# Kernel optimization log

Hardware: AMD Instinct MI355X
Metric: run time of the kernel (lower is better)

Reference implementation:

```python
import jax, jax.numpy as jnp
import numpy as np
import math

B, C, H, W = 32, 384, 64, 64      # batch, backbone dim, feature-map HxW
E, NH = 256, 16                   # embed_dim, num_heads (grapsules per image)
HD = E // NH                      # head dim
RFF_HALF, HID = 32, 128           # RFF rows (out=64), GNN hidden


def setup_inputs() -> dict:
    key = jax.random.key(0)
    ks = jax.random.split(key, 10)
    rn = lambda k, s: (0.02 * jax.random.normal(k, s)).astype(jnp.float32)
    x = jax.random.normal(ks[0], (B, C, H, W), jnp.float32)
    qw = rn(ks[1], (E, C)); qb = jnp.zeros((E,), jnp.float32)
    kw = rn(ks[2], (E, C)); kb = jnp.zeros((E,), jnp.float32)
    vw = rn(ks[3], (E, C)); vb = jnp.zeros((E,), jnp.float32)
    # RFF B ~ N(0,1) * sigma * 2*pi, sigma=1.0
    B_rff = (jax.random.normal(ks[4], (RFF_HALF, 2)) * (2.0 * math.pi)).astype(jnp.float32)
    msg_w = rn(ks[5], (HID, E)); msg_b = jnp.zeros((HID,), jnp.float32)
    emb_w = rn(ks[6], (HID, 2 * RFF_HALF))
    lin1_w = rn(ks[7], (4 * HID, HID)); lin1_b = jnp.zeros((4 * HID,), jnp.float32)
    lin2_w = rn(ks[8], (E, 4 * HID)); lin2_b = jnp.zeros((E,), jnp.float32)
    layer_scale = jnp.full((1, E), 1e-6, jnp.float32)
    # fully-connected directed graph (no self loops) among the NH grapsules of each image
    pairs = np.array([(i, j) for i in range(NH) for j in range(NH) if i != j], dtype=np.int32)
    off = (np.arange(B, dtype=np.int32) * NH)[:, None]
    edge_src = jnp.asarray((pairs[:, 0][None, :] + off).reshape(-1))
    edge_dst = jnp.asarray((pairs[:, 1][None, :] + off).reshape(-1))
    return dict(x=x, qw=qw, qb=qb, kw=kw, kb=kb, vw=vw, vb=vb, B_rff=B_rff,
                msg_w=msg_w, msg_b=msg_b, emb_w=emb_w, lin1_w=lin1_w, lin1_b=lin1_b,
                lin2_w=lin2_w, lin2_b=lin2_b, layer_scale=layer_scale,
                edge_src=edge_src, edge_dst=edge_dst)


def _forward(x, qw, qb, kw, kb, vw, vb, B_rff, msg_w, msg_b, emb_w,
             lin1_w, lin1_b, lin2_w, lin2_b, layer_scale, edge_src, edge_dst):
    Bsz, Cc, Hh, Ww = x.shape
    N = Hh * Ww
    # --- ImageToGraphTransformer (attention pooling to grapsule nodes) ---
    xf = x.reshape(Bsz, Cc, N).transpose(0, 2, 1)            # [B,N,C]
    xm = xf.mean(axis=1)                                     # [B,C]
    q = (xm @ qw.T + qb).reshape(Bsz, NH, HD)                # [B,h,d]
    k = (xf @ kw.T + kb).reshape(Bsz, N, NH, HD)             # [B,N,h,d]
    v = xf @ vw.T + vb                                       # [B,N,E]
    logits = jnp.einsum('bhc,bnhc->bnh', q, k) / math.sqrt(HD)
    attn = jax.nn.softmax(logits, axis=1)                    # softmax over pixels
    xx, yy = jnp.meshgrid(jnp.arange(Hh, dtype=x.dtype), jnp.arange(Ww, dtype=x.dtype), indexing='ij')
    pos_grid = jnp.stack((xx.reshape(-1), yy.reshape(-1)), axis=-1)  # [N,2]
    values = jnp.einsum('bnh,bnc->bhc', attn, v).reshape(Bsz * NH, E)
    pos = jnp.einsum('bnh,nx->bhx', attn, pos_grid).reshape(Bsz * NH, 2)
    # --- RFF embedding of relative positions (edge_attr) ---
    rel = pos[edge_src] - pos[edge_dst]                      # [Eg,2]
    proj = rel @ B_rff.T                                     # [Eg,32]
    edge_attr = math.sqrt(2.0) * jnp.concatenate((jnp.sin(proj), jnp.cos(proj)), axis=-1)
    # --- Conv (MessagePassing) with ConditionalLinear 'strong', mean aggr ---
    m = (values[edge_src] @ msg_w.T + msg_b) * (edge_attr @ emb_w.T)   # [Eg,HID]
    agg = jax.ops.segment_sum(m, edge_dst, num_segments=Bsz * NH) / (NH - 1)
    # --- ConvBlockNeXt MLP + layer scale + identity skip (in==out) ---
    h = jax.nn.silu(agg @ lin1_w.T + lin1_b)
    o = h @ lin2_w.T + lin2_b
    return layer_scale * o + values


def reference(x, qw, qb, kw, kb, vw, vb, B_rff, msg_w, msg_b, emb_w,
              lin1_w, lin1_b, lin2_w, lin2_b, layer_scale, edge_src, edge_dst):
    return _forward(x, qw, qb, kw, kb, vw, vb, B_rff, msg_w, msg_b, emb_w,
                    lin1_w, lin1_b, lin2_w, lin2_b, layer_scale, edge_src, edge_dst)
```

## Files before the change

kernel.cpp:

```cpp
#include <hip/hip_runtime.h>
#include <math.h>


#define Bsz 32
#define Cc  384
#define Nn  4096
#define Ee  256
#define NHh 16
#define HDd 16
#define HIDh 128

__device__ __forceinline__ float waveSum(float v){
#pragma unroll
  for(int o=32;o;o>>=1) v += __shfl_down(v,(unsigned)o,64);
  return v;
}
__device__ __forceinline__ float waveMax(float v){
#pragma unroll
  for(int o=32;o;o>>=1) v = fmaxf(v, __shfl_down(v,(unsigned)o,64));
  return v;
}
__device__ __forceinline__ float blockSum(float v, float* sm){
  int lane = threadIdx.x & 63, w = threadIdx.x >> 6;
  int nw = blockDim.x >> 6;
  float r = waveSum(v);
  if(lane==0) sm[w] = r;
  __syncthreads();
  float s = 0.f;
  for(int i=0;i<nw;i++) s += sm[i];
  __syncthreads();
  return s;
}
__device__ __forceinline__ float blockMax(float v, float* sm){
  int lane = threadIdx.x & 63, w = threadIdx.x >> 6;
  int nw = blockDim.x >> 6;
  float r = waveMax(v);
  if(lane==0) sm[w] = r;
  __syncthreads();
  float s = -1e30f;
  for(int i=0;i<nw;i++) s = fmaxf(s, sm[i]);
  __syncthreads();
  return s;
}

__global__ __launch_bounds__(256) void k_mean(const float* __restrict__ x, float* __restrict__ xm){
  int bc = blockIdx.x, t = threadIdx.x;
  const float4* xr = (const float4*)(x + (size_t)bc*Nn);
  float s = 0.f;
#pragma unroll
  for(int i=0;i<4;i++){ float4 v = xr[t + 256*i]; s += (v.x+v.y) + (v.z+v.w); }
  __shared__ float sm[8];
  s = blockSum(s, sm);
  if(t==0) xm[bc] = s * (1.0f/4096.0f);
}

__global__ __launch_bounds__(384) void k_qk(const float* __restrict__ xm, const float* __restrict__ qw,
                                            const float* __restrict__ qb, const float* __restrict__ kw,
                                            float* __restrict__ qk_t){
  int b = blockIdx.x, t = threadIdx.x;
  __shared__ float xs[Cc];
  __shared__ float qs[Ee];
  if(t < 96) ((float4*)xs)[t] = ((const float4*)(xm + b*Cc))[t];
  __syncthreads();
  if(t < Ee){
    const float4* wr = (const float4*)(qw + (size_t)t*Cc);
    const float4* xv = (const float4*)xs;
    float a = qb[t];
#pragma unroll 4
    for(int c4=0;c4<96;c4++){ float4 w = wr[c4], xx = xv[c4]; a += w.x*xx.x + w.y*xx.y + w.z*xx.z + w.w*xx.w; }
    qs[t] = a;
  }
  __syncthreads();
  int c = t;
#pragma unroll
  for(int hq=0; hq<4; hq++){
    float r0, r1, r2, r3;
#pragma unroll
    for(int hh=0; hh<4; hh++){
      int h = hq*4 + hh;
      float a = 0.f;
#pragma unroll
      for(int d=0; d<16; d++) a += qs[h*16+d] * kw[(size_t)(h*16+d)*Cc + c];
      a *= 0.25f;
      if(hh==0) r0=a; else if(hh==1) r1=a; else if(hh==2) r2=a; else r3=a;
    }
    ((float4*)(qk_t + ((size_t)b*Cc + c)*16))[hq] = make_float4(r0,r1,r2,r3);
  }
}

__global__ __launch_bounds__(256) void k_logits(const float* __restrict__ x, const float* __restrict__ qk_t,
                                                float* __restrict__ lg){
  int b = blockIdx.y;
  int n = blockIdx.x*256 + threadIdx.x;
  float acc[16];
#pragma unroll
  for(int h=0;h<16;h++) acc[h] = 0.f;
  const float* xb = x + (size_t)b*Cc*Nn;
  const float4* qk = (const float4*)(qk_t + (size_t)b*Cc*16);
#pragma unroll 8
  for(int c=0;c<Cc;c++){
    float xv = xb[(size_t)c*Nn + n];
    float4 q0 = qk[c*4+0], q1 = qk[c*4+1], q2 = qk[c*4+2], q3 = qk[c*4+3];
    acc[0]  += xv*q0.x; acc[1]  += xv*q0.y; acc[2]  += xv*q0.z; acc[3]  += xv*q0.w;
    acc[4]  += xv*q1.x; acc[5]  += xv*q1.y; acc[6]  += xv*q1.z; acc[7]  += xv*q1.w;
    acc[8]  += xv*q2.x; acc[9]  += xv*q2.y; acc[10] += xv*q2.z; acc[11] += xv*q2.w;
    acc[12] += xv*q3.x; acc[13] += xv*q3.y; acc[14] += xv*q3.z; acc[15] += xv*q3.w;
  }
#pragma unroll
  for(int h=0;h<16;h++) lg[((size_t)(b*16+h))*Nn + n] = acc[h];
}

__global__ __launch_bounds__(256) void k_softmax(float* __restrict__ lg, float* __restrict__ pos){
  int node = blockIdx.x, t = threadIdx.x;
  __shared__ float sm[8];
  float4* gv = (float4*)(lg + (size_t)node*Nn);
  float4 vv[4];
  float m = -1e30f;
#pragma unroll
  for(int i=0;i<4;i++){
    vv[i] = gv[t + 256*i];
    m = fmaxf(m, fmaxf(fmaxf(vv[i].x, vv[i].y), fmaxf(vv[i].z, vv[i].w)));
  }
  m = blockMax(m, sm);
  float s = 0.f, px = 0.f, py = 0.f;
  float4 ev[4];
#pragma unroll
  for(int i=0;i<4;i++){
    int n0 = 4*(t + 256*i);
    float e0 = __expf(vv[i].x - m), e1 = __expf(vv[i].y - m);
    float e2 = __expf(vv[i].z - m), e3 = __expf(vv[i].w - m);
    float row = (float)(n0 >> 6);
    float c0  = (float)(n0 & 63);
    float es  = (e0+e1)+(e2+e3);
    s  += es;
    px += es * row;
    py += e0*c0 + e1*(c0+1.f) + e2*(c0+2.f) + e3*(c0+3.f);
    ev[i] = make_float4(e0,e1,e2,e3);
  }
  s  = blockSum(s,  sm);
  px = blockSum(px, sm);
  py = blockSum(py, sm);
  float inv = 1.0f / s;
#pragma unroll
  for(int i=0;i<4;i++)
    gv[t + 256*i] = make_float4(ev[i].x*inv, ev[i].y*inv, ev[i].z*inv, ev[i].w*inv);
  if(t==0){ pos[node*2] = px*inv; pos[node*2+1] = py*inv; }
}

#define XROW 36
__global__ __launch_bounds__(256) void k_xa(const float* __restrict__ x, const float* __restrict__ attn,
                                            float* __restrict__ part){
  __shared__ float xl[Cc*XROW];
  __shared__ float al[NHh*XROW];
  int b = blockIdx.y, ns = blockIdx.x, t = threadIdx.x;
  int th = t & 3, tc = t >> 2;
  float acc[4][6];
#pragma unroll
  for(int k=0;k<4;k++)
#pragma unroll
    for(int m=0;m<6;m++) acc[k][m] = 0.f;

  float4 xr[12];
  float4 ar = make_float4(0,0,0,0);
  int ah = t >> 3, aj = t & 7;

  auto LOAD = [&](int ch){
    int n0 = ns*256 + ch*32;
    if(t < 128)
      ar = *(const float4*)(attn + ((size_t)(b*16+ah))*Nn + n0 + aj*4);
#pragma unroll
    for(int i=0;i<12;i++){
      int f = t + 256*i;
      int c = f >> 3, j4 = f & 7;
      xr[i] = *(const float4*)(x + ((size_t)(b*Cc+c))*Nn + n0 + j4*4);
    }
  };

  LOAD(0);
  for(int ch=0; ch<8; ch++){
    if(t < 128) *(float4*)(al + ah*XROW + aj*4) = ar;
#pragma unroll
    for(int i=0;i<12;i++){
      int f = t + 256*i;
      int c = f >> 3, j4 = f & 7;
      *(float4*)(xl + c*XROW + j4*4) = xr[i];
    }
    __syncthreads();
    if(ch < 7) LOAD(ch+1);
#pragma unroll
    for(int j4=0;j4<8;j4++){
      float4 a4[4], x4[6];
#pragma unroll
      for(int k=0;k<4;k++) a4[k] = *(const float4*)(al + (th+4*k)*XROW + j4*4);
#pragma unroll
      for(int m=0;m<6;m++) x4[m] = *(const float4*)(xl + (tc+64*m)*XROW + j4*4);
#pragma unroll
      for(int k=0;k<4;k++)
#pragma unroll
        for(int m=0;m<6;m++)
          acc[k][m] += a4[k].x*x4[m].x + a4[k].y*x4[m].y + a4[k].z*x4[m].z + a4[k].w*x4[m].w;
    }
    __syncthreads();
  }
#pragma unroll
  for(int k=0;k<4;k++)
#pragma unroll
    for(int m=0;m<6;m++)
      part[(size_t)ns*(Bsz*NHh*Cc) + (size_t)(b*16 + th + 4*k)*Cc + (tc + 64*m)] = acc[k][m];
}

__global__ __launch_bounds__(256) void k_values(const float* __restrict__ part, const float* __restrict__ vw,
                                                const float* __restrict__ vb, const float* __restrict__ msg_w,
                                                const float* __restrict__ msg_b,
                                                float* __restrict__ values, float* __restrict__ msgv){
  int node = blockIdx.x, t = threadIdx.x;
  __shared__ float xa[Cc];
  __shared__ float vs[Ee];
  if(t < 96){
    float4 s = make_float4(0,0,0,0);
#pragma unroll
    for(int p=0;p<16;p++){
      float4 v = *(const float4*)(part + (size_t)p*(Bsz*NHh*Cc) + (size_t)node*Cc + t*4);
      s.x += v.x; s.y += v.y; s.z += v.z; s.w += v.w;
    }
    *(float4*)(xa + t*4) = s;
  }
  __syncthreads();
  {
    const float4* wr = (const float4*)(vw + (size_t)t*Cc);
    const float4* xv = (const float4*)xa;
    float a = vb[t];
#pragma unroll 4
    for(int c4=0;c4<96;c4++){ float4 w = wr[c4], xx = xv[c4]; a += w.x*xx.x + w.y*xx.y + w.z*xx.z + w.w*xx.w; }
    values[(size_t)node*Ee + t] = a;
    vs[t] = a;
  }
  __syncthreads();
  if(t < HIDh){
    const float4* mr = (const float4*)(msg_w + (size_t)t*Ee);
    const float4* vv = (const float4*)vs;
    float a = msg_b[t];
#pragma unroll 4
    for(int e4=0;e4<64;e4++){ float4 w = mr[e4], xx = vv[e4]; a += w.x*xx.x + w.y*xx.y + w.z*xx.z + w.w*xx.w; }
    msgv[(size_t)node*HIDh + t] = a;
  }
}

__global__ __launch_bounds__(128) void k_agg(const float* __restrict__ pos, const float* __restrict__ msgv,
                                             const float* __restrict__ brff, const float* __restrict__ emb_w,
                                             float* __restrict__ agg){
  int node = blockIdx.x, t = threadIdx.x;
  int b = node >> 4, jj = node & 15;
  __shared__ float ps[32];
  __shared__ float bf[64];
  __shared__ float mv[16*HIDh];
  __shared__ float ea[64];
  if(t < 32) ps[t] = pos[b*32 + t];
  if(t < 64) bf[t] = brff[t];
#pragma unroll
  for(int i=0;i<4;i++){ int f = t + 128*i; ((float4*)mv)[f] = ((const float4*)(msgv + (size_t)b*16*HIDh))[f]; }
  float4 er[16];
#pragma unroll
  for(int i=0;i<16;i++) er[i] = ((const float4*)(emb_w + (size_t)t*64))[i];
  __syncthreads();
  float pxj = ps[jj*2], pyj = ps[jj*2+1];
  float acc = 0.f;
  for(int i=0;i<16;i++){
    if(i == jj) continue;
    float rx = ps[i*2]   - pxj;
    float ry = ps[i*2+1] - pyj;
    __syncthreads();
    if(t < 32){
      float pr = rx*bf[t*2] + ry*bf[t*2+1];
      ea[t]    = 1.41421356f * __sinf(pr);
      ea[t+32] = 1.41421356f * __cosf(pr);
    }
    __syncthreads();
    float psi = 0.f;
    const float4* eav = (const float4*)ea;
#pragma unroll
    for(int k=0;k<16;k++){ float4 e4 = eav[k]; psi += e4.x*er[k].x + e4.y*er[k].y + e4.z*er[k].z + e4.w*er[k].w; }
    acc += mv[i*HIDh + t] * psi;
  }
  agg[(size_t)node*HIDh + t] = acc * (1.0f/15.0f);
}

__global__ __launch_bounds__(256) void k_mlp(const float* __restrict__ agg, const float* __restrict__ l1w,
                                             const float* __restrict__ l1b, const float* __restrict__ l2w,
                                             const float* __restrict__ l2b, const float* __restrict__ ls,
                                             const float* __restrict__ values, float* __restrict__ out){
  int node = blockIdx.x, t = threadIdx.x;
  __shared__ float ag[HIDh];
  __shared__ float h1[512];
  if(t < 32) ((float4*)ag)[t] = ((const float4*)(agg + (size_t)node*HIDh))[t];
  __syncthreads();
#pragma unroll
  for(int r=0;r<2;r++){
    int u = t + r*256;
    const float4* wr = (const float4*)(l1w + (size_t)u*HIDh);
    const float4* av = (const float4*)ag;
    float a = l1b[u];
#pragma unroll 4
    for(int k=0;k<32;k++){ float4 w = wr[k], xx = av[k]; a += w.x*xx.x + w.y*xx.y + w.z*xx.z + w.w*xx.w; }
    h1[u] = a / (1.0f + __expf(-a));
  }
  __syncthreads();
  {
    const float4* wr = (const float4*)(l2w + (size_t)t*512);
    const float4* hv = (const float4*)h1;
    float o = l2b[t];
#pragma unroll 4
    for(int k=0;k<128;k++){ float4 w = wr[k], xx = hv[k]; o += w.x*xx.x + w.y*xx.y + w.z*xx.z + w.w*xx.w; }
    size_t oi = (size_t)node*Ee + t;
    out[oi] = ls[t]*o + values[oi];
  }
}

extern "C" void kernel_launch(void* const* d_in, const int* in_sizes, int n_in,
                              void* d_out, int out_size, void* d_ws, size_t ws_size,
                              hipStream_t stream) {
  const float* x    = (const float*)d_in[0];
  const float* qw   = (const float*)d_in[1];
  const float* qb   = (const float*)d_in[2];
  const float* kw   = (const float*)d_in[3];
  const float* vw   = (const float*)d_in[5];
  const float* vb   = (const float*)d_in[6];
  const float* brff = (const float*)d_in[7];
  const float* msgw = (const float*)d_in[8];
  const float* msgb = (const float*)d_in[9];
  const float* embw = (const float*)d_in[10];
  const float* l1w  = (const float*)d_in[11];
  const float* l1b  = (const float*)d_in[12];
  const float* l2w  = (const float*)d_in[13];
  const float* l2b  = (const float*)d_in[14];
  const float* lsc  = (const float*)d_in[15];

  float* W      = (float*)d_ws;
  float* xm     = W;
  float* qkt    = xm  + 12288;
  float* lg     = qkt + 196608;
  float* pos    = lg  + 2097152;
  float* part   = pos + 1024;
  float* values = part + 3145728;
  float* msgv   = values + 131072;
  float* agg    = msgv + 65536;
  float* out    = (float*)d_out;

  k_mean   <<<Bsz*Cc, 256, 0, stream>>>(x, xm);
  k_qk     <<<Bsz, 384, 0, stream>>>(xm, qw, qb, kw, qkt);
  k_logits <<<dim3(16, Bsz), 256, 0, stream>>>(x, qkt, lg);
  k_softmax<<<Bsz*NHh, 256, 0, stream>>>(lg, pos);
  k_xa     <<<dim3(16, Bsz), 256, 0, stream>>>(x, lg, part);
  k_values <<<Bsz*NHh, 256, 0, stream>>>(part, vw, vb, msgw, msgb, values, msgv);
  k_agg    <<<Bsz*NHh, 128, 0, stream>>>(pos, msgv, brff, embw, agg);
  k_mlp    <<<Bsz*NHh, 256, 0, stream>>>(agg, l1w, l1b, l2w, l2b, lsc, values, out);
}
```

Before: 580.4 us.

## Fuse tail kernels per image, defer softmax normalization, and retile logits

The logits kernel now stages qk in shared memory and computes two pixels per thread, using half as many blocks. The softmax kernel no longer writes normalized probabilities back. It stores the max and inverse sum, and k_xa applies exp and normalization as it loads attention. The values, agg and MLP kernels are merged into one per-image kernel that processes 16 nodes per block, reusing weights across nodes in register tiles. This trades launch overhead and intermediate global traffic for only 32 blocks in the tail, which lowers parallelism there.

```diff
diff --git a/kernel.cpp b/kernel.cpp
--- a/kernel.cpp
+++ b/kernel.cpp
@@ -7,7 +7,6 @@
 #define Nn  4096
 #define Ee  256
 #define NHh 16
-#define HDd 16
 #define HIDh 128
 
 __device__ __forceinline__ float waveSum(float v){
@@ -90,30 +89,43 @@
 
 __global__ __launch_bounds__(256) void k_logits(const float* __restrict__ x, const float* __restrict__ qk_t,
                                                 float* __restrict__ lg){
-  int b = blockIdx.y;
-  int n = blockIdx.x*256 + threadIdx.x;
-  float acc[16];
-#pragma unroll
-  for(int h=0;h<16;h++) acc[h] = 0.f;
-  const float* xb = x + (size_t)b*Cc*Nn;
-  const float4* qk = (const float4*)(qk_t + (size_t)b*Cc*16);
-#pragma unroll 8
+  __shared__ float qks[Cc*16];
+  int b = blockIdx.y, t = threadIdx.x;
+  int n0 = blockIdx.x*512 + t*2;
+  {
+    const float4* src = (const float4*)(qk_t + (size_t)b*Cc*16);
+    float4* dst = (float4*)qks;
+#pragma unroll
+    for(int i=0;i<6;i++) dst[t + 256*i] = src[t + 256*i];
+  }
+  __syncthreads();
+  float accx[16], accy[16];
+#pragma unroll
+  for(int h=0;h<16;h++){ accx[h]=0.f; accy[h]=0.f; }
+  const float* xb = x + (size_t)b*Cc*Nn + n0;
+#pragma unroll 4
   for(int c=0;c<Cc;c++){
-    float xv = xb[(size_t)c*Nn + n];
-    float4 q0 = qk[c*4+0], q1 = qk[c*4+1], q2 = qk[c*4+2], q3 = qk[c*4+3];
-    acc[0]  += xv*q0.x; acc[1]  += xv*q0.y; acc[2]  += xv*q0.z; acc[3]  += xv*q0.w;
-    acc[4]  += xv*q1.x; acc[5]  += xv*q1.y; acc[6]  += xv*q1.z; acc[7]  += xv*q1.w;
-    acc[8]  += xv*q2.x; acc[9]  += xv*q2.y; acc[10] += xv*q2.z; acc[11] += xv*q2.w;
-    acc[12] += xv*q3.x; acc[13] += xv*q3.y; acc[14] += xv*q3.z; acc[15] += xv*q3.w;
-  }
-#pragma unroll
-  for(int h=0;h<16;h++) lg[((size_t)(b*16+h))*Nn + n] = acc[h];
-}
-
-__global__ __launch_bounds__(256) void k_softmax(float* __restrict__ lg, float* __restrict__ pos){
+    float2 xv = *(const float2*)(xb + (size_t)c*Nn);
+    const float4* qv = (const float4*)(qks + c*16);
+#pragma unroll
+    for(int hq=0;hq<4;hq++){
+      float4 q = qv[hq];
+      accx[hq*4+0] += xv.x*q.x; accy[hq*4+0] += xv.y*q.x;
+      accx[hq*4+1] += xv.x*q.y; accy[hq*4+1] += xv.y*q.y;
+      accx[hq*4+2] += xv.x*q.z; accy[hq*4+2] += xv.y*q.z;
+      accx[hq*4+3] += xv.x*q.w; accy[hq*4+3] += xv.y*q.w;
+    }
+  }
+#pragma unroll
+  for(int h=0;h<16;h++)
+    *(float2*)(lg + ((size_t)(b*16+h))*Nn + n0) = make_float2(accx[h], accy[h]);
+}
+
+__global__ __launch_bounds__(256) void k_stats(const float* __restrict__ lg, float* __restrict__ pos,
+                                               float* __restrict__ stats){
   int node = blockIdx.x, t = threadIdx.x;
   __shared__ float sm[8];
-  float4* gv = (float4*)(lg + (size_t)node*Nn);
+  const float4* gv = (const float4*)(lg + (size_t)node*Nn);
   float4 vv[4];
   float m = -1e30f;
 #pragma unroll
@@ -123,7 +135,6 @@
   }
   m = blockMax(m, sm);
   float s = 0.f, px = 0.f, py = 0.f;
-  float4 ev[4];
 #pragma unroll
   for(int i=0;i<4;i++){
     int n0 = 4*(t + 256*i);
@@ -135,25 +146,32 @@
     s  += es;
     px += es * row;
     py += e0*c0 + e1*(c0+1.f) + e2*(c0+2.f) + e3*(c0+3.f);
-    ev[i] = make_float4(e0,e1,e2,e3);
   }
   s  = blockSum(s,  sm);
   px = blockSum(px, sm);
   py = blockSum(py, sm);
   float inv = 1.0f / s;
-#pragma unroll
-  for(int i=0;i<4;i++)
-    gv[t + 256*i] = make_float4(ev[i].x*inv, ev[i].y*inv, ev[i].z*inv, ev[i].w*inv);
-  if(t==0){ pos[node*2] = px*inv; pos[node*2+1] = py*inv; }
+  if(t==0){
+    pos[node*2]   = px*inv;
+    pos[node*2+1] = py*inv;
+    stats[node*2]   = m;
+    stats[node*2+1] = inv;
+  }
 }
 
 #define XROW 36
-__global__ __launch_bounds__(256) void k_xa(const float* __restrict__ x, const float* __restrict__ attn,
-                                            float* __restrict__ part){
+__global__ __launch_bounds__(256) void k_xa(const float* __restrict__ x, const float* __restrict__ lg,
+                                            const float* __restrict__ stats, float* __restrict__ part){
   __shared__ float xl[Cc*XROW];
   __shared__ float al[NHh*XROW];
+  __shared__ float ss[32];
   int b = blockIdx.y, ns = blockIdx.x, t = threadIdx.x;
   int th = t & 3, tc = t >> 2;
+  if(t < 32) ss[t] = stats[b*32 + t];
+  __syncthreads();
+  int ah = t >> 3, aj = t & 7;
+  float mA = 0.f, iA = 0.f;
+  if(t < 128){ mA = ss[ah*2]; iA = ss[ah*2+1]; }
   float acc[4][6];
 #pragma unroll
   for(int k=0;k<4;k++)
@@ -162,12 +180,11 @@
 
   float4 xr[12];
   float4 ar = make_float4(0,0,0,0);
-  int ah = t >> 3, aj = t & 7;
 
   auto LOAD = [&](int ch){
     int n0 = ns*256 + ch*32;
     if(t < 128)
-      ar = *(const float4*)(attn + ((size_t)(b*16+ah))*Nn + n0 + aj*4);
+      ar = *(const float4*)(lg + ((size_t)(b*16+ah))*Nn + n0 + aj*4);
 #pragma unroll
     for(int i=0;i<12;i++){
       int f = t + 256*i;
@@ -178,7 +195,14 @@
 
   LOAD(0);
   for(int ch=0; ch<8; ch++){
-    if(t < 128) *(float4*)(al + ah*XROW + aj*4) = ar;
+    if(t < 128){
+      float4 e;
+      e.x = __expf(ar.x - mA)*iA;
+      e.y = __expf(ar.y - mA)*iA;
+      e.z = __expf(ar.z - mA)*iA;
+      e.w = __expf(ar.w - mA)*iA;
+      *(float4*)(al + ah*XROW + aj*4) = e;
+    }
 #pragma unroll
     for(int i=0;i<12;i++){
       int f = t + 256*i;
@@ -209,110 +233,190 @@
       part[(size_t)ns*(Bsz*NHh*Cc) + (size_t)(b*16 + th + 4*k)*Cc + (tc + 64*m)] = acc[k][m];
 }
 
-__global__ __launch_bounds__(256) void k_values(const float* __restrict__ part, const float* __restrict__ vw,
-                                                const float* __restrict__ vb, const float* __restrict__ msg_w,
-                                                const float* __restrict__ msg_b,
-                                                float* __restrict__ values, float* __restrict__ msgv){
-  int node = blockIdx.x, t = threadIdx.x;
-  __shared__ float xa[Cc];
-  __shared__ float vs[Ee];
-  if(t < 96){
+__global__ __launch_bounds__(256) void k_tail(const float* __restrict__ part,
+        const float* __restrict__ vw, const float* __restrict__ vb,
+        const float* __restrict__ msgw, const float* __restrict__ msgb,
+        const float* __restrict__ pos, const float* __restrict__ brff,
+        const float* __restrict__ embw,
+        const float* __restrict__ l1w, const float* __restrict__ l1b,
+        const float* __restrict__ l2w, const float* __restrict__ l2b,
+        const float* __restrict__ ls, float* __restrict__ out){
+  __shared__ float u1[16*516];
+  __shared__ float vs[16*260];
+  __shared__ float ag[16*132];
+  __shared__ float ps[32];
+  __shared__ float bfs[64];
+  float* xa = u1;
+  float* mg = u1;
+  float* ea = u1 + 2112;
+  float* h1 = u1;
+  int b = blockIdx.x, t = threadIdx.x;
+  int w = t >> 6, lane = t & 63;
+
+#pragma unroll
+  for(int i=0;i<6;i++){
+    int idx = t + 256*i;
+    int j = idx / 96, c4 = idx % 96;
     float4 s = make_float4(0,0,0,0);
+    const float* base = part + (size_t)(b*16+j)*Cc + c4*4;
 #pragma unroll
     for(int p=0;p<16;p++){
-      float4 v = *(const float4*)(part + (size_t)p*(Bsz*NHh*Cc) + (size_t)node*Cc + t*4);
-      s.x += v.x; s.y += v.y; s.z += v.z; s.w += v.w;
-    }
-    *(float4*)(xa + t*4) = s;
-  }
-  __syncthreads();
-  {
-    const float4* wr = (const float4*)(vw + (size_t)t*Cc);
-    const float4* xv = (const float4*)xa;
-    float a = vb[t];
-#pragma unroll 4
-    for(int c4=0;c4<96;c4++){ float4 w = wr[c4], xx = xv[c4]; a += w.x*xx.x + w.y*xx.y + w.z*xx.z + w.w*xx.w; }
-    values[(size_t)node*Ee + t] = a;
-    vs[t] = a;
-  }
-  __syncthreads();
-  if(t < HIDh){
-    const float4* mr = (const float4*)(msg_w + (size_t)t*Ee);
-    const float4* vv = (const float4*)vs;
-    float a = msg_b[t];
-#pragma unroll 4
-    for(int e4=0;e4<64;e4++){ float4 w = mr[e4], xx = vv[e4]; a += w.x*xx.x + w.y*xx.y + w.z*xx.z + w.w*xx.w; }
-    msgv[(size_t)node*HIDh + t] = a;
-  }
-}
-
-__global__ __launch_bounds__(128) void k_agg(const float* __restrict__ pos, const float* __restrict__ msgv,
-                                             const float* __restrict__ brff, const float* __restrict__ emb_w,
-                                             float* __restrict__ agg){
-  int node = blockIdx.x, t = threadIdx.x;
-  int b = node >> 4, jj = node & 15;
-  __shared__ float ps[32];
-  __shared__ float bf[64];
-  __shared__ float mv[16*HIDh];
-  __shared__ float ea[64];
+      float4 v = *(const float4*)(base + (size_t)p*(Bsz*NHh*Cc));
+      s.x+=v.x; s.y+=v.y; s.z+=v.z; s.w+=v.w;
+    }
+    *(float4*)(xa + j*388 + c4*4) = s;
+  }
   if(t < 32) ps[t] = pos[b*32 + t];
-  if(t < 64) bf[t] = brff[t];
-#pragma unroll
-  for(int i=0;i<4;i++){ int f = t + 128*i; ((float4*)mv)[f] = ((const float4*)(msgv + (size_t)b*16*HIDh))[f]; }
-  float4 er[16];
-#pragma unroll
-  for(int i=0;i<16;i++) er[i] = ((const float4*)(emb_w + (size_t)t*64))[i];
-  __syncthreads();
-  float pxj = ps[jj*2], pyj = ps[jj*2+1];
-  float acc = 0.f;
-  for(int i=0;i<16;i++){
-    if(i == jj) continue;
-    float rx = ps[i*2]   - pxj;
-    float ry = ps[i*2+1] - pyj;
+  if(t < 64) bfs[t] = brff[t];
+  __syncthreads();
+
+  {
+    float acc[4][4];
+#pragma unroll
+    for(int jj=0;jj<4;jj++)
+#pragma unroll
+      for(int ee=0;ee<4;ee++) acc[jj][ee] = 0.f;
+    for(int c4=0;c4<96;c4++){
+      float4 w4[4], a4[4];
+#pragma unroll
+      for(int ee=0;ee<4;ee++) w4[ee] = *(const float4*)(vw + (size_t)(lane+64*ee)*Cc + c4*4);
+#pragma unroll
+      for(int jj=0;jj<4;jj++) a4[jj] = *(const float4*)(xa + (w*4+jj)*388 + c4*4);
+#pragma unroll
+      for(int jj=0;jj<4;jj++)
+#pragma unroll
+        for(int ee=0;ee<4;ee++)
+          acc[jj][ee] += a4[jj].x*w4[ee].x + a4[jj].y*w4[ee].y + a4[jj].z*w4[ee].z + a4[jj].w*w4[ee].w;
+    }
     __syncthreads();
-    if(t < 32){
-      float pr = rx*bf[t*2] + ry*bf[t*2+1];
-      ea[t]    = 1.41421356f * __sinf(pr);
-      ea[t+32] = 1.41421356f * __cosf(pr);
+#pragma unroll
+    for(int jj=0;jj<4;jj++)
+#pragma unroll
+      for(int ee=0;ee<4;ee++)
+        vs[(w*4+jj)*260 + lane+64*ee] = acc[jj][ee] + vb[lane+64*ee];
+  }
+  __syncthreads();
+
+  {
+    float acc[4][2];
+#pragma unroll
+    for(int jj=0;jj<4;jj++){ acc[jj][0]=0.f; acc[jj][1]=0.f; }
+    for(int e4=0;e4<64;e4++){
+      float4 w4[2], v4[4];
+#pragma unroll
+      for(int hh=0;hh<2;hh++) w4[hh] = *(const float4*)(msgw + (size_t)(lane+64*hh)*Ee + e4*4);
+#pragma unroll
+      for(int jj=0;jj<4;jj++) v4[jj] = *(const float4*)(vs + (w*4+jj)*260 + e4*4);
+#pragma unroll
+      for(int jj=0;jj<4;jj++)
+#pragma unroll
+        for(int hh=0;hh<2;hh++)
+          acc[jj][hh] += v4[jj].x*w4[hh].x + v4[jj].y*w4[hh].y + v4[jj].z*w4[hh].z + v4[jj].w*w4[hh].w;
+    }
+#pragma unroll
+    for(int jj=0;jj<4;jj++)
+#pragma unroll
+      for(int hh=0;hh<2;hh++)
+        mg[(w*4+jj)*132 + lane+64*hh] = acc[jj][hh] + msgb[lane+64*hh];
+  }
+  __syncthreads();
+
+  {
+    int h = t & 127;
+    int jbase = (t >> 7) * 8;
+    float4 er[16];
+#pragma unroll
+    for(int k=0;k<16;k++) er[k] = *(const float4*)(embw + (size_t)h*64 + k*4);
+    float accJ[8];
+#pragma unroll
+    for(int jl=0;jl<8;jl++) accJ[jl] = 0.f;
+    for(int i=0;i<16;i++){
+      __syncthreads();
+      {
+        int j = t >> 4, kk = (t & 15)*2;
+        float rx = ps[2*i]   - ps[2*j];
+        float ry = ps[2*i+1] - ps[2*j+1];
+#pragma unroll
+        for(int u=0;u<2;u++){
+          int k = kk + u;
+          float pr = rx*bfs[2*k] + ry*bfs[2*k+1];
+          ea[j*68 + k]      = 1.41421356f * __sinf(pr);
+          ea[j*68 + 32 + k] = 1.41421356f * __cosf(pr);
+        }
+      }
+      __syncthreads();
+      float mvh = mg[i*132 + h];
+#pragma unroll
+      for(int jl=0;jl<8;jl++){
+        int j = jbase + jl;
+        if(j == i) continue;
+        float psi = 0.f;
+        const float4* ev = (const float4*)(ea + j*68);
+#pragma unroll
+        for(int k=0;k<16;k++){ float4 e4 = ev[k]; psi += e4.x*er[k].x + e4.y*er[k].y + e4.z*er[k].z + e4.w*er[k].w; }
+        accJ[jl] += mvh * psi;
+      }
     }
     __syncthreads();
-    float psi = 0.f;
-    const float4* eav = (const float4*)ea;
-#pragma unroll
-    for(int k=0;k<16;k++){ float4 e4 = eav[k]; psi += e4.x*er[k].x + e4.y*er[k].y + e4.z*er[k].z + e4.w*er[k].w; }
-    acc += mv[i*HIDh + t] * psi;
-  }
-  agg[(size_t)node*HIDh + t] = acc * (1.0f/15.0f);
-}
-
-__global__ __launch_bounds__(256) void k_mlp(const float* __restrict__ agg, const float* __restrict__ l1w,
-                                             const float* __restrict__ l1b, const float* __restrict__ l2w,
-                                             const float* __restrict__ l2b, const float* __restrict__ ls,
-                                             const float* __restrict__ values, float* __restrict__ out){
-  int node = blockIdx.x, t = threadIdx.x;
-  __shared__ float ag[HIDh];
-  __shared__ float h1[512];
-  if(t < 32) ((float4*)ag)[t] = ((const float4*)(agg + (size_t)node*HIDh))[t];
-  __syncthreads();
-#pragma unroll
-  for(int r=0;r<2;r++){
-    int u = t + r*256;
-    const float4* wr = (const float4*)(l1w + (size_t)u*HIDh);
-    const float4* av = (const float4*)ag;
-    float a = l1b[u];
-#pragma unroll 4
-    for(int k=0;k<32;k++){ float4 w = wr[k], xx = av[k]; a += w.x*xx.x + w.y*xx.y + w.z*xx.z + w.w*xx.w; }
-    h1[u] = a / (1.0f + __expf(-a));
-  }
-  __syncthreads();
-  {
-    const float4* wr = (const float4*)(l2w + (size_t)t*512);
-    const float4* hv = (const float4*)h1;
-    float o = l2b[t];
-#pragma unroll 4
-    for(int k=0;k<128;k++){ float4 w = wr[k], xx = hv[k]; o += w.x*xx.x + w.y*xx.y + w.z*xx.z + w.w*xx.w; }
-    size_t oi = (size_t)node*Ee + t;
-    out[oi] = ls[t]*o + values[oi];
+#pragma unroll
+    for(int jl=0;jl<8;jl++) ag[(jbase+jl)*132 + h] = accJ[jl] * (1.0f/15.0f);
+  }
+  __syncthreads();
+
+  {
+    float acc[4][8];
+#pragma unroll
+    for(int jj=0;jj<4;jj++)
+#pragma unroll
+      for(int uu=0;uu<8;uu++) acc[jj][uu] = 0.f;
+    for(int c4=0;c4<32;c4++){
+      float4 w4[8], a4[4];
+#pragma unroll
+      for(int uu=0;uu<8;uu++) w4[uu] = *(const float4*)(l1w + (size_t)(lane+64*uu)*HIDh + c4*4);
+#pragma unroll
+      for(int jj=0;jj<4;jj++) a4[jj] = *(const float4*)(ag + (w*4+jj)*132 + c4*4);
+#pragma unroll
+      for(int jj=0;jj<4;jj++)
+#pragma unroll
+        for(int uu=0;uu<8;uu++)
+          acc[jj][uu] += a4[jj].x*w4[uu].x + a4[jj].y*w4[uu].y + a4[jj].z*w4[uu].z + a4[jj].w*w4[uu].w;
+    }
+#pragma unroll
+    for(int jj=0;jj<4;jj++)
+#pragma unroll
+      for(int uu=0;uu<8;uu++){
+        float a = acc[jj][uu] + l1b[lane+64*uu];
+        h1[(w*4+jj)*516 + lane+64*uu] = a / (1.0f + __expf(-a));
+      }
+  }
+  __syncthreads();
+
+  {
+    float acc[4][4];
+#pragma unroll
+    for(int jj=0;jj<4;jj++)
+#pragma unroll
+      for(int ee=0;ee<4;ee++) acc[jj][ee] = 0.f;
+    for(int u4=0;u4<128;u4++){
+      float4 w4[4], hv[4];
+#pragma unroll
+      for(int ee=0;ee<4;ee++) w4[ee] = *(const float4*)(l2w + (size_t)(lane+64*ee)*512 + u4*4);
+#pragma unroll
+      for(int jj=0;jj<4;jj++) hv[jj] = *(const float4*)(h1 + (w*4+jj)*516 + u4*4);
+#pragma unroll
+      for(int jj=0;jj<4;jj++)
+#pragma unroll
+        for(int ee=0;ee<4;ee++)
+          acc[jj][ee] += hv[jj].x*w4[ee].x + hv[jj].y*w4[ee].y + hv[jj].z*w4[ee].z + hv[jj].w*w4[ee].w;
+    }
+#pragma unroll
+    for(int jj=0;jj<4;jj++)
+#pragma unroll
+      for(int ee=0;ee<4;ee++){
+        int e = lane + 64*ee;
+        size_t oi = (size_t)(b*16 + w*4+jj)*Ee + e;
+        out[oi] = ls[e]*(acc[jj][ee] + l2b[e]) + vs[(w*4+jj)*260 + e];
+      }
   }
 }
 
@@ -340,18 +444,15 @@
   float* qkt    = xm  + 12288;
   float* lg     = qkt + 196608;
   float* pos    = lg  + 2097152;
-  float* part   = pos + 1024;
-  float* values = part + 3145728;
-  float* msgv   = values + 131072;
-  float* agg    = msgv + 65536;
+  float* stats  = pos + 1024;
+  float* part   = stats + 1024;
   float* out    = (float*)d_out;
 
-  k_mean   <<<Bsz*Cc, 256, 0, stream>>>(x, xm);
-  k_qk     <<<Bsz, 384, 0, stream>>>(xm, qw, qb, kw, qkt);
-  k_logits <<<dim3(16, Bsz), 256, 0, stream>>>(x, qkt, lg);
-  k_softmax<<<Bsz*NHh, 256, 0, stream>>>(lg, pos);
-  k_xa     <<<dim3(16, Bsz), 256, 0, stream>>>(x, lg, part);
-  k_values <<<Bsz*NHh, 256, 0, stream>>>(part, vw, vb, msgw, msgb, values, msgv);
-  k_agg    <<<Bsz*NHh, 128, 0, stream>>>(pos, msgv, brff, embw, agg);
-  k_mlp    <<<Bsz*NHh, 256, 0, stream>>>(agg, l1w, l1b, l2w, l2b, lsc, values, out);
-}
+  k_mean  <<<Bsz*Cc, 256, 0, stream>>>(x, xm);
+  k_qk    <<<Bsz, 384, 0, stream>>>(xm, qw, qb, kw, qkt);
+  k_logits<<<dim3(8, Bsz), 256, 0, stream>>>(x, qkt, lg);
+  k_stats <<<Bsz*NHh, 256, 0, stream>>>(lg, pos, stats);
+  k_xa    <<<dim3(16, Bsz), 256, 0, stream>>>(x, lg, stats, part);
+  k_tail  <<<Bsz, 256, 0, stream>>>(part, vw, vb, msgw, msgb, pos, brff, embw,
+                                    l1w, l1b, l2w, l2b, lsc, out);
+}
```

Result: slower. 714.8 us (+23.1%).
